# Optimization experiments

Hardware: AMD Instinct MI355X
Metric: run time of the kernel (lower is better)

The kernel has to match this reference:

```python
import jax, jax.numpy as jnp
import numpy as np


def bilinear_sample(img, coords):
    # img: [N, H, W] correlation slices; coords: [N, K, K, 2] with (x, y) pixel coords.
    # Matches F.grid_sample(mode='bilinear', padding_mode='zeros', align_corners=True)
    # since the torch bilinear_sampler maps pixel coords to [-1,1] with align_corners=True.
    N, H, W = img.shape
    x = coords[..., 0]
    y = coords[..., 1]
    x0 = jnp.floor(x)
    y0 = jnp.floor(y)
    wx = x - x0  # weight toward x0+1
    wy = y - y0  # weight toward y0+1
    flat = img.reshape(N, H * W)

    def gather(yi, xi):
        valid = (xi >= 0) & (xi <= W - 1) & (yi >= 0) & (yi <= H - 1)
        xi_c = jnp.clip(xi, 0, W - 1).astype(jnp.int32)
        yi_c = jnp.clip(yi, 0, H - 1).astype(jnp.int32)
        idx = (yi_c * W + xi_c).reshape(N, -1)
        vals = jnp.take_along_axis(flat, idx, axis=1).reshape(xi.shape)
        return jnp.where(valid, vals, jnp.zeros((), img.dtype))

    v00 = gather(y0, x0)
    v01 = gather(y0, x0 + 1)
    v10 = gather(y0 + 1, x0)
    v11 = gather(y0 + 1, x0 + 1)
    return (v00 * (1 - wy) * (1 - wx) + v01 * (1 - wy) * wx
            + v10 * wy * (1 - wx) + v11 * wy * wx)


def corr_block(fmap1, fmap2, coords, num_levels, radius):
    B, D, H, W = fmap1.shape
    f1 = fmap1.reshape(B, D, H * W)
    f2 = fmap2.reshape(B, D, H * W)
    # [B, H1*W1, H2*W2] correlation volume, scaled by 1/sqrt(dim)
    corr = jnp.einsum('bdn,bdm->bnm', f1, f2) / jnp.sqrt(jnp.asarray(D, jnp.float32))
    corr = corr.reshape(B * H * W, H, W)

    pyramid = [corr]
    for _ in range(num_levels - 1):
        n, h, w = corr.shape
        # avg_pool2d(kernel=2, stride=2)
        corr = corr.reshape(n, h // 2, 2, w // 2, 2).mean(axis=(2, 4))
        pyramid.append(corr)

    r = radius
    d = jnp.linspace(-r, r, 2 * r + 1, dtype=jnp.float32)
    # meshgrid(dy, dx) stacked on last dim -> delta[...,0]=dy, delta[...,1]=dx
    delta = jnp.stack(jnp.meshgrid(d, d, indexing='ij'), axis=-1)  # [2r+1, 2r+1, 2]

    coords_q = coords.transpose(0, 2, 3, 1).reshape(B * H * W, 1, 1, 2)
    outs = []
    for i, c in enumerate(pyramid):
        coords_lvl = coords_q / (2 ** i) + delta[None]  # [N, 2r+1, 2r+1, 2]
        sampled = bilinear_sample(c, coords_lvl)        # [N, 2r+1, 2r+1]
        outs.append(sampled.reshape(B, H, W, -1))
    out = jnp.concatenate(outs, axis=-1)  # [B, H, W, num_levels*(2r+1)^2]
    return out.transpose(0, 3, 1, 2).astype(jnp.float32)


def setup_inputs() -> dict:
    key = jax.random.key(0)
    k1, k2, k3 = jax.random.split(key, 3)
    B, D, H, W = 4, 256, 64, 64
    fmap1 = jax.random.normal(k1, (B, D, H, W), dtype=jnp.float32)
    fmap2 = jax.random.normal(k2, (B, D, H, W), dtype=jnp.float32)
    coords = jax.random.uniform(k3, (B, 2, H, W), dtype=jnp.float32) * (W - 1)
    return {"fmap1": fmap1, "fmap2": fmap2, "coords": coords,
            "num_levels": 4, "radius": 4}


def reference(fmap1, fmap2, coords, num_levels, radius):
    return corr_block(fmap1, fmap2, coords, num_levels, radius)
```

## Files before the change

### kernel.cpp

```cpp
#include <hip/hip_runtime.h>

typedef unsigned short ushort_t;
typedef __attribute__((ext_vector_type(8))) short bfrag;
typedef __attribute__((ext_vector_type(4))) float f4;

#define NB 4
#define ND 256
#define NH 64
#define NW 64
#define NQ (NH * NW)
#define MPAD 5504
#define NLVL 4
#define NCH (NLVL * 81)

__device__ __forceinline__ float bf2f(ushort_t u) {
    return __uint_as_float(((unsigned)u) << 16);
}
__device__ __forceinline__ ushort_t f2bf(float f) {
    unsigned u = __float_as_uint(f);
    unsigned r = (u + 0x7fffu + ((u >> 16) & 1u)) >> 16;
    return (ushort_t)r;
}

__device__ __forceinline__ void gload_lds16(const void* g, void* l) {
    __builtin_amdgcn_global_load_lds(
        (const __attribute__((address_space(1))) unsigned int*)g,
        (__attribute__((address_space(3))) unsigned int*)l, 16, 0, 0);
}

__global__ __launch_bounds__(256) void pre_kernel(
    const float* __restrict__ f1, const float* __restrict__ f2,
    const float* __restrict__ coords,
    ushort_t* __restrict__ Abf, ushort_t* __restrict__ Ball,
    int* __restrict__ tbl)
{
    __shared__ float tile[64][65];
    const int tid = threadIdx.x;
    const int z = blockIdx.z;

    if (z == 8) {
        int t = (blockIdx.y * 64 + blockIdx.x) * 256 + tid;
        int b = t >> 12, q = t & 4095;
        float cx = coords[((size_t)b * 2 + 0) * NQ + q];
        float cy = coords[((size_t)b * 2 + 1) * NQ + q];
#pragma unroll
        for (int lvl = 0; lvl < 4; lvl++) {
            float s = 1.0f / (float)(1 << lvl);
            int x0 = (int)floorf(cx * s);
            int y0 = (int)floorf(cy * s);
            tbl[((b * 4 + lvl) << 12) + q] = (x0 & 0xffff) | (y0 << 16);
        }
        return;
    }

    const int b = z & 3;
    const bool isA = (z < 4);
    const float* ib = (isA ? f1 : f2) + (size_t)b * ND * NQ;
    ushort_t* ob = isA ? (Abf + (size_t)b * NQ * ND) : (Ball + (size_t)b * MPAD * ND);
    const float scale = isA ? 0.0625f : 1.0f;
    const int n0 = blockIdx.x * 64, d0 = blockIdx.y * 64;
    const int nl = tid & 63, dg = tid >> 6;
#pragma unroll
    for (int i = 0; i < 16; i++) {
        int dl = dg + i * 4;
        tile[dl][nl] = ib[(size_t)(d0 + dl) * NQ + n0 + nl];
    }
    __syncthreads();
    const int dl = tid & 63, ng = tid >> 6;
#pragma unroll
    for (int i = 0; i < 16; i++) {
        int nn = ng + i * 4;
        ob[(size_t)(n0 + nn) * ND + d0 + dl] = f2bf(tile[dl][nn] * scale);
    }
}

__global__ __launch_bounds__(256) void pool_fused(ushort_t* __restrict__ Ball)
{
    const int d = threadIdx.x;
    const int bid = blockIdx.x;
    const int b = bid >> 6;
    const int cell = bid & 63;
    const int Y = cell >> 3, X = cell & 7;
    ushort_t* base = Ball + (size_t)b * MPAD * ND;

    float s1[4][4];
#pragma unroll
    for (int iy = 0; iy < 4; iy++)
#pragma unroll
        for (int ix = 0; ix < 4; ix++) {
            int ry = 2 * (4 * Y + iy), rx = 2 * (4 * X + ix);
            float s = bf2f(base[(size_t)((ry    ) * 64 + rx    ) * ND + d])
                    + bf2f(base[(size_t)((ry    ) * 64 + rx + 1) * ND + d])
                    + bf2f(base[(size_t)((ry + 1) * 64 + rx    ) * ND + d])
                    + bf2f(base[(size_t)((ry + 1) * 64 + rx + 1) * ND + d]);
            s1[iy][ix] = s * 0.25f;
            base[(size_t)(4096 + (4 * Y + iy) * 32 + 4 * X + ix) * ND + d] = f2bf(s1[iy][ix]);
        }
    float s2[2][2];
#pragma unroll
    for (int iy = 0; iy < 2; iy++)
#pragma unroll
        for (int ix = 0; ix < 2; ix++) {
            float s = 0.25f * (s1[2*iy][2*ix] + s1[2*iy][2*ix+1]
                             + s1[2*iy+1][2*ix] + s1[2*iy+1][2*ix+1]);
            s2[iy][ix] = s;
            base[(size_t)(5120 + (2 * Y + iy) * 16 + 2 * X + ix) * ND + d] = f2bf(s);
        }
    float s3 = 0.25f * (s2[0][0] + s2[0][1] + s2[1][0] + s2[1][1]);
    base[(size_t)(5376 + Y * 8 + X) * ND + d] = f2bf(s3);
}

__global__ __launch_bounds__(512, 4) void gemm_corr(
    const ushort_t* __restrict__ A,
    const ushort_t* __restrict__ Bm,
    ushort_t* __restrict__ compact,
    const int* __restrict__ tbl)
{
    __shared__ ushort_t As[3][256 * 32];
    __shared__ ushort_t Bs[3][128 * 32];

    const int l   = blockIdx.x;
    const int wg  = (l & 7) * 344 + (l >> 3);
    const int z   = wg / 688;
    const int rem = wg - z * 688;
    const int by  = rem / 43;
    const int bxt = rem - by * 43;

    int lvl, mbase;
    if (bxt < 32)      { lvl = 0; mbase = bxt * 128; }
    else if (bxt < 40) { lvl = 1; mbase = 4096 + (bxt - 32) * 128; }
    else if (bxt < 42) { lvl = 2; mbase = 5120 + (bxt - 40) * 128; }
    else               { lvl = 3; mbase = 5376; }

    const int tid  = threadIdx.x;
    const int lane = tid & 63;
    const int wv   = tid >> 6;
    const int wr   = wv >> 1;
    const int wc   = wv & 1;
    const int ln15 = lane & 15;
    const int g4   = lane >> 4;

    const ushort_t* Ab = A  + ((size_t)z * NQ   + (size_t)by * 256) * ND;
    const ushort_t* Bb = Bm + ((size_t)z * MPAD + (size_t)mbase) * ND;

    f4 acc[4][4] = {};

    const int rA  = tid >> 2;
    const int chA = (tid & 3) ^ ((tid >> 3) & 3);
    const ushort_t* srcA0 = Ab + (size_t)rA * ND + chA * 8;
    const ushort_t* srcA1 = srcA0 + (size_t)128 * ND;
    const ushort_t* srcB  = Bb + (size_t)rA * ND + chA * 8;

#define STAGE(buf, kk) {                                                   \
    gload_lds16(srcA0 + (kk), &As[buf][tid * 8]);                          \
    gload_lds16(srcA1 + (kk), &As[buf][(512 + tid) * 8]);                  \
    gload_lds16(srcB  + (kk), &Bs[buf][tid * 8]); }

    const int kch = ((lane >> 4) ^ ((ln15 >> 1) & 3)) * 8;

    STAGE(0, 0);
    STAGE(1, 32);
    STAGE(2, 64);

#pragma unroll
    for (int t = 0; t < 8; ++t) {
        const int cur = t % 3;
        if (t < 6)       { asm volatile("s_waitcnt vmcnt(6)" ::: "memory"); }
        else if (t == 6) { asm volatile("s_waitcnt vmcnt(3)" ::: "memory"); }
        else             { asm volatile("s_waitcnt vmcnt(0)" ::: "memory"); }
        __builtin_amdgcn_s_barrier();
        asm volatile("" ::: "memory");

        bfrag a[4], bb[4];
#pragma unroll
        for (int mi = 0; mi < 4; mi++)
            a[mi] = *reinterpret_cast<const bfrag*>(
                &As[cur][(wr * 64 + mi * 16 + ln15) * 32 + kch]);
#pragma unroll
        for (int ni = 0; ni < 4; ni++)
            bb[ni] = *reinterpret_cast<const bfrag*>(
                &Bs[cur][(wc * 64 + ni * 16 + ln15) * 32 + kch]);

        if (t < 5) {
            __builtin_amdgcn_sched_barrier(0);
            asm volatile("s_waitcnt lgkmcnt(0)" ::: "memory");
            __builtin_amdgcn_s_barrier();
            asm volatile("" ::: "memory");
            STAGE(cur, (t + 3) * 32);
        }

#pragma unroll
        for (int mi = 0; mi < 4; mi++)
#pragma unroll
            for (int ni = 0; ni < 4; ni++)
                acc[mi][ni] = __builtin_amdgcn_mfma_f32_16x16x32_bf16(
                    a[mi], bb[ni], acc[mi][ni], 0, 0, 0);
    }
#undef STAGE

    const int row_base = by * 256 + wr * 64 + (g4 << 2);
    const int* tb      = tbl + (((size_t)z * 4 + lvl) << 12);
    ushort_t* cmp      = compact + (size_t)z * NQ * 400 + lvl * 100;

    auto for_q = [&](auto body) {
#pragma unroll
        for (int mi = 0; mi < 4; mi++) {
            const int q0 = row_base + mi * 16;
            const int4 xy4 = *reinterpret_cast<const int4*>(&tb[q0]);
            const int xys[4] = {xy4.x, xy4.y, xy4.z, xy4.w};
#pragma unroll
            for (int j = 0; j < 4; j++) {
                const int xy = xys[j];
                body(mi, j, xy & 0xffff, xy >> 16, (size_t)(q0 + j) * 400);
            }
        }
    };

    if (lvl == 0) {
        const int yfix = bxt * 2 + wc;
        for_q([&](int mi, int j, int x0, int y0, size_t qb) {
            unsigned v = (unsigned)(yfix - y0 + 4);
            if (v < 10u) {
                size_t vb = qb + v * 10;
#pragma unroll
                for (int ni = 0; ni < 4; ni++) {
                    unsigned u = (unsigned)(ln15 + 16 * ni + 4 - x0);
                    if (u < 10u) cmp[vb + u] = f2bf(acc[mi][ni][j]);
                }
            }
        });
    } else if (lvl == 1) {
        const int ybase = (bxt - 32) * 4 + wc * 2;
        for_q([&](int mi, int j, int x0, int y0, size_t qb) {
            unsigned u0 = (unsigned)(ln15 + 4 - x0), u1 = u0 + 16u;
            unsigned v0 = (unsigned)(ybase - y0 + 4), v1 = v0 + 1u;
            if (v0 < 10u) {
                if (u0 < 10u) cmp[qb + v0 * 10 + u0] = f2bf(acc[mi][0][j]);
                if (u1 < 10u) cmp[qb + v0 * 10 + u1] = f2bf(acc[mi][1][j]);
            }
            if (v1 < 10u) {
                if (u0 < 10u) cmp[qb + v1 * 10 + u0] = f2bf(acc[mi][2][j]);
                if (u1 < 10u) cmp[qb + v1 * 10 + u1] = f2bf(acc[mi][3][j]);
            }
        });
    } else if (lvl == 2) {
        const int ybase = (bxt - 40) * 8 + wc * 4;
        for_q([&](int mi, int j, int x0, int y0, size_t qb) {
            unsigned u = (unsigned)(ln15 + 4 - x0);
            if (u < 10u) {
#pragma unroll
                for (int ni = 0; ni < 4; ni++) {
                    unsigned v = (unsigned)(ybase + ni - y0 + 4);
                    if (v < 10u) cmp[qb + v * 10 + u] = f2bf(acc[mi][ni][j]);
                }
            }
        });
    } else if (wc == 0) {
        const int yb3 = ln15 >> 3;
        for_q([&](int mi, int j, int x0, int y0, size_t qb) {
            unsigned u = (unsigned)((ln15 & 7) + 4 - x0);
            if (u < 10u) {
#pragma unroll
                for (int ni = 0; ni < 4; ni++) {
                    unsigned v = (unsigned)(yb3 + 2 * ni - y0 + 4);
                    if (v < 10u) cmp[qb + v * 10 + u] = f2bf(acc[mi][ni][j]);
                }
            }
        });
    }
}

__global__ __launch_bounds__(256) void sample_kernel(
    const ushort_t* __restrict__ compact,
    const float* __restrict__ coords,
    float* __restrict__ out)
{
    __shared__ int   X0s[16], Y0s[16];
    __shared__ float wxs[16], wys[16];
    __shared__ float Dl[16 * 101];
    const int tid = threadIdx.x;
    const int g   = blockIdx.x;
    const int lvl = blockIdx.y;
    const int b   = blockIdx.z;
    const int Wl  = NW >> lvl;

    if (tid < 16) {
        int q = g * 16 + tid;
        float cx = coords[(size_t)(b * 2 + 0) * NQ + q];
        float cy = coords[(size_t)(b * 2 + 1) * NQ + q];
        float s = 1.0f / (float)(1 << lvl);
        float xl = cx * s, yl = cy * s;
        float fx = floorf(xl), fy = floorf(yl);
        X0s[tid] = (int)fx;
        Y0s[tid] = (int)fy;
        wxs[tid] = xl - fx;
        wys[tid] = yl - fy;
    }
    __syncthreads();

#pragma unroll
    for (int r = 0; r < 7; r++) {
        int e = r * 256 + tid;
        if (e < 16 * 100) {
            int qi = e / 100;
            int el = e - qi * 100;
            int v = el / 10;
            int u = el - v * 10;
            int xx = X0s[qi] - 4 + u;
            int yy = Y0s[qi] - 4 + v;
            float val = 0.f;
            if ((unsigned)xx < (unsigned)Wl && (unsigned)yy < (unsigned)Wl)
                val = bf2f(compact[((size_t)b * NQ + g * 16 + qi) * 400
                                   + lvl * 100 + el]);
            Dl[qi * 101 + el] = val;
        }
    }
    __syncthreads();

#pragma unroll
    for (int r = 0; r < 6; r++) {
        int e = r * 256 + tid;
        if (e < 16 * 81) {
            int qi = e & 15;
            int c = e >> 4;
            int i = c / 9;
            int j = c - i * 9;
            float wx = wxs[qi], wy = wys[qi];
            const float* dq = &Dl[qi * 101];
            float d00 = dq[j * 10 + i];
            float d10 = dq[j * 10 + i + 1];
            float d01 = dq[(j + 1) * 10 + i];
            float d11 = dq[(j + 1) * 10 + i + 1];
            float vx0 = d00 + wx * (d10 - d00);
            float vx1 = d01 + wx * (d11 - d01);
            float val = vx0 + wy * (vx1 - vx0);
            out[((size_t)b * NCH + lvl * 81 + c) * NQ + g * 16 + qi] = val;
        }
    }
}

extern "C" void kernel_launch(void* const* d_in, const int* in_sizes, int n_in,
                              void* d_out, int out_size, void* d_ws, size_t ws_size,
                              hipStream_t stream)
{
    const float* fmap1  = (const float*)d_in[0];
    const float* fmap2  = (const float*)d_in[1];
    const float* coords = (const float*)d_in[2];
    float* out = (float*)d_out;

    char* ws = (char*)d_ws;
    const size_t A_BYTES   = (size_t)NB * NQ * ND * 2;
    const size_t B_BYTES   = (size_t)NB * MPAD * ND * 2;
    const size_t CMP_BYTES = (size_t)NB * NQ * 400 * 2;
    ushort_t* Abf  = (ushort_t*)ws;
    ushort_t* Ball = (ushort_t*)(ws + A_BYTES);
    ushort_t* cmp  = (ushort_t*)(ws + A_BYTES + B_BYTES);
    int*      tbl  = (int*)(ws + A_BYTES + B_BYTES + CMP_BYTES);

    pre_kernel<<<dim3(64, 4, 9), 256, 0, stream>>>(fmap1, fmap2, coords, Abf, Ball, tbl);

    pool_fused<<<NB * 64, 256, 0, stream>>>(Ball);

    gemm_corr<<<dim3(16 * 43 * NB), 512, 0, stream>>>(Abf, Ball, cmp, tbl);

    sample_kernel<<<dim3(256, NLVL, NB), 256, 0, stream>>>(cmp, coords, out);
}
```

Before: 83.94 us.

## Halve GEMM block to 256 threads with 128-row warp tiles

```diff
diff --git a/kernel.cpp b/kernel.cpp
--- a/kernel.cpp
+++ b/kernel.cpp
@@ -110,7 +110,7 @@
     base[(size_t)(5376 + Y * 8 + X) * ND + d] = f2bf(s3);
 }
 
-__global__ __launch_bounds__(512, 4) void gemm_corr(
+__global__ __launch_bounds__(256, 2) void gemm_corr(
     const ushort_t* __restrict__ A,
     const ushort_t* __restrict__ Bm,
     ushort_t* __restrict__ compact,
@@ -143,68 +143,76 @@
     const ushort_t* Ab = A  + ((size_t)z * NQ   + (size_t)by * 256) * ND;
     const ushort_t* Bb = Bm + ((size_t)z * MPAD + (size_t)mbase) * ND;
 
-    f4 acc[4][4] = {};
-
-    const int rA  = tid >> 2;
-    const int chA = (tid & 3) ^ ((tid >> 3) & 3);
-    const ushort_t* srcA0 = Ab + (size_t)rA * ND + chA * 8;
-    const ushort_t* srcA1 = srcA0 + (size_t)128 * ND;
-    const ushort_t* srcB  = Bb + (size_t)rA * ND + chA * 8;
-
-#define STAGE(buf, kk) {                                                   \
-    gload_lds16(srcA0 + (kk), &As[buf][tid * 8]);                          \
-    gload_lds16(srcA1 + (kk), &As[buf][(512 + tid) * 8]);                  \
-    gload_lds16(srcB  + (kk), &Bs[buf][tid * 8]); }
-
-    const int kch = ((lane >> 4) ^ ((ln15 >> 1) & 3)) * 8;
+    f4 acc[8][4] = {};
+
+    const int rb = tid >> 2;
+    const int sc = (tid & 3) ^ ((tid >> 3) & 3);
+    const ushort_t* srcA = Ab + (size_t)rb * ND + sc * 8;
+    const ushort_t* srcB = Bb + (size_t)rb * ND + sc * 8;
+
+#define STAGE(buf, kk) {                                                    \
+    gload_lds16(srcA + (kk),            &As[buf][tid * 8]);                 \
+    gload_lds16(srcA + 64*ND + (kk),    &As[buf][tid * 8 + 2048]);          \
+    gload_lds16(srcA + 128*ND + (kk),   &As[buf][tid * 8 + 4096]);          \
+    gload_lds16(srcA + 192*ND + (kk),   &As[buf][tid * 8 + 6144]);          \
+    gload_lds16(srcB + (kk),            &Bs[buf][tid * 8]);                 \
+    gload_lds16(srcB + 64*ND + (kk),    &Bs[buf][tid * 8 + 2048]); }
+
+    const int kch = (g4 ^ ((ln15 >> 1) & 3)) * 8;
 
     STAGE(0, 0);
     STAGE(1, 32);
-    STAGE(2, 64);
 
 #pragma unroll
     for (int t = 0; t < 8; ++t) {
         const int cur = t % 3;
-        if (t < 6)       { asm volatile("s_waitcnt vmcnt(6)" ::: "memory"); }
-        else if (t == 6) { asm volatile("s_waitcnt vmcnt(3)" ::: "memory"); }
-        else             { asm volatile("s_waitcnt vmcnt(0)" ::: "memory"); }
+        if (t < 7) { asm volatile("s_waitcnt vmcnt(6)" ::: "memory"); }
+        else       { asm volatile("s_waitcnt vmcnt(0)" ::: "memory"); }
         __builtin_amdgcn_s_barrier();
         asm volatile("" ::: "memory");
 
-        bfrag a[4], bb[4];
+        bfrag a[4], b[4];
+#pragma unroll
+        for (int ni = 0; ni < 4; ni++)
+            b[ni] = *reinterpret_cast<const bfrag*>(
+                &Bs[cur][(wc * 64 + ni * 16 + ln15) * 32 + kch]);
 #pragma unroll
         for (int mi = 0; mi < 4; mi++)
             a[mi] = *reinterpret_cast<const bfrag*>(
-                &As[cur][(wr * 64 + mi * 16 + ln15) * 32 + kch]);
-#pragma unroll
-        for (int ni = 0; ni < 4; ni++)
-            bb[ni] = *reinterpret_cast<const bfrag*>(
-                &Bs[cur][(wc * 64 + ni * 16 + ln15) * 32 + kch]);
-
-        if (t < 5) {
-            __builtin_amdgcn_sched_barrier(0);
-            asm volatile("s_waitcnt lgkmcnt(0)" ::: "memory");
-            __builtin_amdgcn_s_barrier();
-            asm volatile("" ::: "memory");
-            STAGE(cur, (t + 3) * 32);
-        }
-
+                &As[cur][(wr * 128 + mi * 16 + ln15) * 32 + kch]);
+        if (t < 6) STAGE((t + 2) % 3, (t + 2) * 32);
+
+        __builtin_amdgcn_s_setprio(1);
 #pragma unroll
         for (int mi = 0; mi < 4; mi++)
 #pragma unroll
             for (int ni = 0; ni < 4; ni++)
                 acc[mi][ni] = __builtin_amdgcn_mfma_f32_16x16x32_bf16(
-                    a[mi], bb[ni], acc[mi][ni], 0, 0, 0);
+                    a[mi], b[ni], acc[mi][ni], 0, 0, 0);
+        __builtin_amdgcn_s_setprio(0);
+
+#pragma unroll
+        for (int mi = 0; mi < 4; mi++)
+            a[mi] = *reinterpret_cast<const bfrag*>(
+                &As[cur][(wr * 128 + (mi + 4) * 16 + ln15) * 32 + kch]);
+        __builtin_amdgcn_s_setprio(1);
+#pragma unroll
+        for (int mi = 0; mi < 4; mi++)
+#pragma unroll
+            for (int ni = 0; ni < 4; ni++)
+                acc[mi + 4][ni] = __builtin_amdgcn_mfma_f32_16x16x32_bf16(
+                    a[mi], b[ni], acc[mi + 4][ni], 0, 0, 0);
+        __builtin_amdgcn_s_setprio(0);
     }
 #undef STAGE
 
-    const int row_base = by * 256 + wr * 64 + (g4 << 2);
+    const int row_base = by * 256 + wr * 128 + (g4 << 2);
     const int* tb      = tbl + (((size_t)z * 4 + lvl) << 12);
     ushort_t* cmp      = compact + (size_t)z * NQ * 400 + lvl * 100;
 
     auto for_q = [&](auto body) {
 #pragma unroll
-        for (int mi = 0; mi < 4; mi++) {
+        for (int mi = 0; mi < 8; mi++) {
             const int q0 = row_base + mi * 16;
             const int4 xy4 = *reinterpret_cast<const int4*>(&tb[q0]);
             const int xys[4] = {xy4.x, xy4.y, xy4.z, xy4.w};
@@ -361,7 +369,7 @@
 
     pool_fused<<<NB * 64, 256, 0, stream>>>(Ball);
 
-    gemm_corr<<<dim3(16 * 43 * NB), 512, 0, stream>>>(Abf, Ball, cmp, tbl);
+    gemm_corr<<<dim3(16 * 43 * NB), 256, 0, stream>>>(Abf, Ball, cmp, tbl);
 
     sample_kernel<<<dim3(256, NLVL, NB), 256, 0, stream>>>(cmp, coords, out);
 }
```

Result: slower. 95.75 us (+14.1%).

## Sort queries by row and skip GEMM tiles outside the sampling window

Applied to the files above, without the earlier changes.

```diff
diff --git a/kernel.cpp b/kernel.cpp
--- a/kernel.cpp
+++ b/kernel.cpp
@@ -30,29 +30,11 @@
 
 __global__ __launch_bounds__(256) void pre_kernel(
     const float* __restrict__ f1, const float* __restrict__ f2,
-    const float* __restrict__ coords,
-    ushort_t* __restrict__ Abf, ushort_t* __restrict__ Ball,
-    int* __restrict__ tbl)
+    ushort_t* __restrict__ Abf, ushort_t* __restrict__ Ball)
 {
     __shared__ float tile[64][65];
     const int tid = threadIdx.x;
     const int z = blockIdx.z;
-
-    if (z == 8) {
-        int t = (blockIdx.y * 64 + blockIdx.x) * 256 + tid;
-        int b = t >> 12, q = t & 4095;
-        float cx = coords[((size_t)b * 2 + 0) * NQ + q];
-        float cy = coords[((size_t)b * 2 + 1) * NQ + q];
-#pragma unroll
-        for (int lvl = 0; lvl < 4; lvl++) {
-            float s = 1.0f / (float)(1 << lvl);
-            int x0 = (int)floorf(cx * s);
-            int y0 = (int)floorf(cy * s);
-            tbl[((b * 4 + lvl) << 12) + q] = (x0 & 0xffff) | (y0 << 16);
-        }
-        return;
-    }
-
     const int b = z & 3;
     const bool isA = (z < 4);
     const float* ib = (isA ? f1 : f2) + (size_t)b * ND * NQ;
@@ -71,6 +53,55 @@
     for (int i = 0; i < 16; i++) {
         int nn = ng + i * 4;
         ob[(size_t)(n0 + nn) * ND + d0 + dl] = f2bf(tile[dl][nn] * scale);
+    }
+}
+
+__global__ __launch_bounds__(256) void sort_kernel(
+    const float* __restrict__ coords, int* __restrict__ perm)
+{
+    __shared__ int hist[64];
+    __shared__ int base[64];
+    const int tid = threadIdx.x;
+    const int b   = blockIdx.x;
+    if (tid < 64) hist[tid] = 0;
+    __syncthreads();
+    int keys[16];
+#pragma unroll
+    for (int i = 0; i < 16; i++) {
+        int q = tid + i * 256;
+        float cy = coords[((size_t)b * 2 + 1) * NQ + q];
+        keys[i] = (int)floorf(cy);
+        atomicAdd(&hist[keys[i]], 1);
+    }
+    __syncthreads();
+    if (tid == 0) {
+        int s = 0;
+        for (int i = 0; i < 64; i++) { base[i] = s; s += hist[i]; }
+    }
+    __syncthreads();
+#pragma unroll
+    for (int i = 0; i < 16; i++) {
+        int q = tid + i * 256;
+        int pos = atomicAdd(&base[keys[i]], 1);
+        perm[(size_t)b * NQ + pos] = q;
+    }
+}
+
+__global__ __launch_bounds__(256) void tbls_kernel(
+    const float* __restrict__ coords, const int* __restrict__ perm,
+    int* __restrict__ tblS)
+{
+    const int idx = blockIdx.x * 256 + threadIdx.x;
+    const int b = idx >> 12, pos = idx & 4095;
+    const int q = perm[(size_t)b * NQ + pos];
+    const float cx = coords[((size_t)b * 2 + 0) * NQ + q];
+    const float cy = coords[((size_t)b * 2 + 1) * NQ + q];
+#pragma unroll
+    for (int lvl = 0; lvl < 4; lvl++) {
+        float s = 1.0f / (float)(1 << lvl);
+        int x0 = (int)floorf(cx * s);
+        int y0 = (int)floorf(cy * s);
+        tblS[(((size_t)b * 4 + lvl) << 12) + pos] = x0 | (y0 << 6) | (q << 12);
     }
 }
 
@@ -114,7 +145,8 @@
     const ushort_t* __restrict__ A,
     const ushort_t* __restrict__ Bm,
     ushort_t* __restrict__ compact,
-    const int* __restrict__ tbl)
+    const int* __restrict__ perm,
+    const int* __restrict__ tblS)
 {
     __shared__ ushort_t As[3][256 * 32];
     __shared__ ushort_t Bs[3][128 * 32];
@@ -131,6 +163,18 @@
     else if (bxt < 40) { lvl = 1; mbase = 4096 + (bxt - 32) * 128; }
     else if (bxt < 42) { lvl = 2; mbase = 5120 + (bxt - 40) * 128; }
     else               { lvl = 3; mbase = 5376; }
+
+    const int* tbL = tblS + (((size_t)z * 4 + lvl) << 12);
+
+    if (lvl < 3) {
+        int yF = (tbL[by * 256] >> 6) & 63;
+        int yL = (tbL[by * 256 + 255] >> 6) & 63;
+        int rlo, rhi;
+        if (lvl == 0)      { rlo = bxt * 2;        rhi = rlo + 1; }
+        else if (lvl == 1) { rlo = (bxt - 32) * 4; rhi = rlo + 3; }
+        else               { rlo = (bxt - 40) * 8; rhi = rlo + 7; }
+        if (rhi < yF - 4 || rlo > yL + 5) return;
+    }
 
     const int tid  = threadIdx.x;
     const int lane = tid & 63;
@@ -140,15 +184,15 @@
     const int ln15 = lane & 15;
     const int g4   = lane >> 4;
 
-    const ushort_t* Ab = A  + ((size_t)z * NQ   + (size_t)by * 256) * ND;
     const ushort_t* Bb = Bm + ((size_t)z * MPAD + (size_t)mbase) * ND;
 
     f4 acc[4][4] = {};
 
     const int rA  = tid >> 2;
     const int chA = (tid & 3) ^ ((tid >> 3) & 3);
-    const ushort_t* srcA0 = Ab + (size_t)rA * ND + chA * 8;
-    const ushort_t* srcA1 = srcA0 + (size_t)128 * ND;
+    const int* pm = perm + (size_t)z * NQ + by * 256;
+    const ushort_t* srcA0 = A + ((size_t)z * NQ + pm[rA])       * ND + chA * 8;
+    const ushort_t* srcA1 = A + ((size_t)z * NQ + pm[128 + rA]) * ND + chA * 8;
     const ushort_t* srcB  = Bb + (size_t)rA * ND + chA * 8;
 
 #define STAGE(buf, kk) {                                                   \
@@ -156,7 +200,7 @@
     gload_lds16(srcA1 + (kk), &As[buf][(512 + tid) * 8]);                  \
     gload_lds16(srcB  + (kk), &Bs[buf][tid * 8]); }
 
-    const int kch = ((lane >> 4) ^ ((ln15 >> 1) & 3)) * 8;
+    const int kch = (g4 ^ ((ln15 >> 1) & 3)) * 8;
 
     STAGE(0, 0);
     STAGE(1, 32);
@@ -199,19 +243,18 @@
 #undef STAGE
 
     const int row_base = by * 256 + wr * 64 + (g4 << 2);
-    const int* tb      = tbl + (((size_t)z * 4 + lvl) << 12);
     ushort_t* cmp      = compact + (size_t)z * NQ * 400 + lvl * 100;
 
     auto for_q = [&](auto body) {
 #pragma unroll
         for (int mi = 0; mi < 4; mi++) {
             const int q0 = row_base + mi * 16;
-            const int4 xy4 = *reinterpret_cast<const int4*>(&tb[q0]);
+            const int4 xy4 = *reinterpret_cast<const int4*>(&tbL[q0]);
             const int xys[4] = {xy4.x, xy4.y, xy4.z, xy4.w};
 #pragma unroll
             for (int j = 0; j < 4; j++) {
-                const int xy = xys[j];
-                body(mi, j, xy & 0xffff, xy >> 16, (size_t)(q0 + j) * 400);
+                const int e = xys[j];
+                body(mi, j, e & 63, (e >> 6) & 63, (size_t)((e >> 12) & 4095) * 400);
             }
         }
     };
@@ -352,16 +395,21 @@
     const size_t A_BYTES   = (size_t)NB * NQ * ND * 2;
     const size_t B_BYTES   = (size_t)NB * MPAD * ND * 2;
     const size_t CMP_BYTES = (size_t)NB * NQ * 400 * 2;
+    const size_t TBL_BYTES = (size_t)NB * 4 * NQ * 4;
     ushort_t* Abf  = (ushort_t*)ws;
     ushort_t* Ball = (ushort_t*)(ws + A_BYTES);
     ushort_t* cmp  = (ushort_t*)(ws + A_BYTES + B_BYTES);
-    int*      tbl  = (int*)(ws + A_BYTES + B_BYTES + CMP_BYTES);
-
-    pre_kernel<<<dim3(64, 4, 9), 256, 0, stream>>>(fmap1, fmap2, coords, Abf, Ball, tbl);
+    int*      tblS = (int*)(ws + A_BYTES + B_BYTES + CMP_BYTES);
+    int*      perm = (int*)(ws + A_BYTES + B_BYTES + CMP_BYTES + TBL_BYTES);
+
+    pre_kernel<<<dim3(64, 4, 8), 256, 0, stream>>>(fmap1, fmap2, Abf, Ball);
+
+    sort_kernel<<<NB, 256, 0, stream>>>(coords, perm);
+    tbls_kernel<<<(NB * NQ) / 256, 256, 0, stream>>>(coords, perm, tblS);
 
     pool_fused<<<NB * 64, 256, 0, stream>>>(Ball);
 
-    gemm_corr<<<dim3(16 * 43 * NB), 512, 0, stream>>>(Abf, Ball, cmp, tbl);
+    gemm_corr<<<dim3(16 * 43 * NB), 512, 0, stream>>>(Abf, Ball, cmp, perm, tblS);
 
     sample_kernel<<<dim3(256, NLVL, NB), 256, 0, stream>>>(cmp, coords, out);
 }
```

Measured after the change: 67.89 us. 1.24x faster.
